# Performance work log

Measured on AMD Instinct MI355X. Metric: run time of the kernel, lower is better.

## Reference

```python
import jax, jax.numpy as jnp
import numpy as np

K = 36  # neighbors

def _gather(points, idx):
    # points: [B,N,C], idx: [B,N,K] -> [B,N,K,C]
    return jax.vmap(lambda p, i: p[i])(points, idx)

def setup_inputs() -> dict:
    key = jax.random.key(0)
    ks = jax.random.split(key, 16)
    B, N, d_points, d_model = 4, 4096, 32, 128
    def lin(k, fan_in, shape):
        return jax.random.normal(k, shape, dtype=jnp.float32) / np.sqrt(fan_in)
    return {
        "features": jax.random.normal(ks[0], (B, N, d_points), dtype=jnp.float32),
        "xyz": jax.random.uniform(ks[1], (B, N, 3), dtype=jnp.float32),
        "W1": lin(ks[2], d_points, (d_model, d_points)), "b1": jnp.zeros((d_model,), jnp.float32),
        "W2": lin(ks[3], d_model, (d_model, d_model)), "b2": jnp.zeros((d_model,), jnp.float32),
        "Wd1": lin(ks[4], 3, (d_model, 3)), "bd1": jnp.zeros((d_model,), jnp.float32),
        "Wd2": lin(ks[5], d_model, (d_model, d_model)), "bd2": jnp.zeros((d_model,), jnp.float32),
        "Wg1": lin(ks[6], d_model, (d_model, d_model)), "bg1": jnp.zeros((d_model,), jnp.float32),
        "Wg2": lin(ks[7], d_model, (d_model, d_model)), "bg2": jnp.zeros((d_model,), jnp.float32),
    }

def reference(features, xyz, W1, b1, W2, b2, Wd1, bd1, Wd2, bd2, Wg1, bg1, Wg2, bg2):
    # square_distance: [B,N,N]
    sq = jnp.sum(xyz * xyz, axis=-1)
    dists = sq[:, :, None] + sq[:, None, :] - 2.0 * jnp.einsum('bnc,bmc->bnm', xyz, xyz)
    knn_idx = jnp.argsort(dists, axis=-1)[:, :, :K]            # [B,N,K]
    knn_xyz = _gather(xyz, knn_idx)                             # [B,N,K,3]
    x = features @ W1.T + b1                                    # [B,N,d]
    k = _gather(x, knn_idx)                                     # [B,N,K,d]
    v = k
    # fc_delta(xyz[:,:,None] - knn_xyz)
    d_in = xyz[:, :, None, :] - knn_xyz                         # [B,N,K,3]
    pos_enc = jax.nn.relu(d_in @ Wd1.T + bd1) @ Wd2.T + bd2     # [B,N,K,d]
    # fc_gamma(q[:,:,None] - k + pos_enc)
    g_in = x[:, :, None, :] - k + pos_enc
    attn_pre = jax.nn.relu(g_in @ Wg1.T + bg1) @ Wg2.T + bg2    # [B,N,K,d]
    attn = jax.nn.softmax(attn_pre / np.sqrt(x.shape[-1]).astype(np.float32), axis=-2)
    res = jnp.einsum('bmnf,bmnf->bmf', attn, v + pos_enc)       # [B,N,d]
    res = res @ W2.T + b2 + x
    return (res, attn)
```

## Files before the change

kernel.cpp:

```cpp
#include <hip/hip_runtime.h>
#include <math.h>

#define BB 4
#define NPT 4096
#define DP 32
#define DD 128
#define KNB 36

typedef unsigned short ushort_t;
typedef unsigned int uint_t;
typedef unsigned long long ull;
typedef __attribute__((ext_vector_type(8))) short bf16x8;
typedef __attribute__((ext_vector_type(4))) float f32x4;

__device__ __forceinline__ ushort_t f2bf(float f) {
    unsigned u = __float_as_uint(f);
    unsigned r = (u + 0x7FFFu + ((u >> 16) & 1u)) >> 16;
    return (ushort_t)r;
}
__device__ __forceinline__ float bf2f(ushort_t h) {
    return __uint_as_float((unsigned)h << 16);
}
__device__ __forceinline__ int swzi(int r, int f) {
    return (r << 7) + (((f >> 3) ^ (r & 15)) << 3) + (f & 7);
}

__global__ __launch_bounds__(256) void k_wcvt(const float* __restrict__ Wd2,
                                              const float* __restrict__ Wg1,
                                              const float* __restrict__ Wg2,
                                              const float* __restrict__ W2,
                                              ushort_t* __restrict__ wb) {
    int i = blockIdx.x * 256 + threadIdx.x;
    wb[i]           = f2bf(Wd2[i]);
    wb[i + 16384]   = f2bf(Wg1[i]);
    wb[i + 32768]   = f2bf(Wg2[i]);
    wb[i + 49152]   = f2bf(W2[i]);
}

__global__ __launch_bounds__(128) void k_x(const float* __restrict__ feat,
                                           const float* __restrict__ xyz,
                                           const float* __restrict__ W1,
                                           const float* __restrict__ b1,
                                           float* __restrict__ x,
                                           float* __restrict__ sq) {
    int row = blockIdx.x;
    int t = threadIdx.x;
    __shared__ float sf[DP];
    if (t < DP) sf[t] = feat[row * DP + t];
    __syncthreads();
    float acc = 0.f;
#pragma unroll
    for (int c = 0; c < DP; ++c) acc = fmaf(sf[c], W1[t * DP + c], acc);
    x[(size_t)row * DD + t] = acc + b1[t];
    if (t == 0) {
        float a = xyz[row * 3 + 0], b = xyz[row * 3 + 1], c = xyz[row * 3 + 2];
        float s = __fadd_rn(__fadd_rn(__fmul_rn(a, a), __fmul_rn(b, b)),
                            __fmul_rn(c, c));
        sq[row] = s;
    }
}

__global__ __launch_bounds__(256) void k_knn2(const float* __restrict__ xyz,
                                              const float* __restrict__ sq,
                                              int* __restrict__ knn) {
    const int row = blockIdx.x;
    const int b = row >> 12;
    const int t = threadIdx.x;
    const int lane = t & 63, wv = t >> 6;

    __shared__ __align__(16) ull cand[2048];
    __shared__ int wsum[4];
    __shared__ ull wred[4];
    __shared__ ull sbest;
    __shared__ int sC, sCnt;

    uint_t* hist4 = (uint_t*)cand;

    const float qx = xyz[row * 3 + 0], qy = xyz[row * 3 + 1], qz = xyz[row * 3 + 2];
    const float qs = sq[row];
    const float* bx = xyz + (size_t)b * NPT * 3;
    const float* bs = sq + (size_t)b * NPT;

#pragma unroll
    for (int i = 0; i < 16; ++i) hist4[t + (i << 8)] = 0;
    if (t == 0) sCnt = 0;
    __syncthreads();

    uint_t k16[16];
#pragma unroll
    for (int i = 0; i < 16; ++i) {
        int m = t + (i << 8);
        float px = bx[m * 3 + 0], py = bx[m * 3 + 1], pz = bx[m * 3 + 2];
        float d0 = __fmul_rn(qx, px);
        float d1 = __fmaf_rn(qy, py, d0);
        float dot = __fmaf_rn(qz, pz, d1);
        float d = __fsub_rn(__fadd_rn(qs, bs[m]), __fmul_rn(2.0f, dot));
        unsigned u = __float_as_uint(d);
        u = (u & 0x80000000u) ? ~u : (u | 0x80000000u);
        k16[i] = u;
        int bin = (u < 0x80000000u) ? 0 : (int)((u - 0x80000000u) >> 21);
        atomicAdd(&hist4[(bin << 2) | (t & 3)], 1u);
    }
    __syncthreads();

    int s_t = 0;
#pragma unroll
    for (int i = 0; i < 16; ++i) s_t += (int)hist4[(t << 4) + i];
    int v = s_t;
    for (int off = 1; off < 64; off <<= 1) {
        int o = __shfl_up(v, off, 64);
        if (lane >= off) v += o;
    }
    if (lane == 63) wsum[wv] = v;
    __syncthreads();
    int base = 0;
    for (int w0 = 0; w0 < wv; ++w0) base += wsum[w0];
    int cumIncl = base + v, cumExcl = cumIncl - s_t;
    if (cumExcl < KNB && cumIncl >= KNB) {
        int run = cumExcl;
#pragma unroll
        for (int j = 0; j < 4; ++j) {
            int bb = (t << 2) + j;
            int h = (int)(hist4[(bb << 2) + 0] + hist4[(bb << 2) + 1] +
                          hist4[(bb << 2) + 2] + hist4[(bb << 2) + 3]);
            if (run + h >= KNB) { sC = bb; break; }
            run += h;
        }
    }
    __syncthreads();
    const int C = sC;

#pragma unroll
    for (int i = 0; i < 16; ++i) {
        uint_t u = k16[i];
        int bin = (u < 0x80000000u) ? 0 : (int)((u - 0x80000000u) >> 21);
        if (bin <= C) {
            int p = atomicAdd(&sCnt, 1);
            if (p < 2048) cand[p] = ((ull)u << 32) | (uint_t)(t + (i << 8));
        }
    }
    __syncthreads();
    const int cnt = sCnt;

    if (cnt <= 64) {
        if (wv == 0) {
            ull x = (lane < cnt) ? cand[lane] : ~0ull;
#pragma unroll
            for (int k = 2; k <= 64; k <<= 1) {
#pragma unroll
                for (int j = k >> 1; j > 0; j >>= 1) {
                    ull o = __shfl_xor(x, j, 64);
                    bool up = ((lane & k) == 0);
                    bool lower = ((lane & j) == 0);
                    ull mn = (x < o) ? x : o;
                    ull mx = (x < o) ? o : x;
                    x = (up == lower) ? mn : mx;
                }
            }
            if (lane < KNB) knn[(size_t)row * KNB + lane] = (int)(x & 0xffffffffu);
        }
        return;
    }

    if (cnt <= 2048) {
        ull lk = ~0ull;
        for (int i = t; i < cnt; i += 256) { ull k = cand[i]; if (k < lk) lk = k; }
        for (int r = 0; r < KNB; ++r) {
            ull k = lk;
#pragma unroll
            for (int off = 32; off >= 1; off >>= 1) {
                ull o = __shfl_down(k, off, 64);
                if (o < k) k = o;
            }
            if (lane == 0) wred[wv] = k;
            __syncthreads();
            if (t == 0) {
                ull best = wred[0];
                for (int w0 = 1; w0 < 4; ++w0) if (wred[w0] < best) best = wred[w0];
                sbest = best;
                knn[(size_t)row * KNB + r] = (int)(best & 0xffffffffu);
            }
            __syncthreads();
            ull best = sbest;
            if (lk == best) {
                for (int i = t; i < cnt; i += 256)
                    if (cand[i] == best) cand[i] = ~0ull;
                ull nm = ~0ull;
                for (int i = t; i < cnt; i += 256) { ull kk = cand[i]; if (kk < nm) nm = kk; }
                lk = nm;
            }
        }
        return;
    }

    {
        uint_t* bm = (uint_t*)cand;
        if (t < 128) bm[t] = 0;
        __syncthreads();
        ull lk = ~0ull;
#pragma unroll
        for (int i = 0; i < 16; ++i) {
            ull k = ((ull)k16[i] << 32) | (uint_t)(t + (i << 8));
            if (k < lk) lk = k;
        }
        for (int r = 0; r < KNB; ++r) {
            ull k = lk;
#pragma unroll
            for (int off = 32; off >= 1; off >>= 1) {
                ull o = __shfl_down(k, off, 64);
                if (o < k) k = o;
            }
            if (lane == 0) wred[wv] = k;
            __syncthreads();
            if (t == 0) {
                ull best = wred[0];
                for (int w0 = 1; w0 < 4; ++w0) if (wred[w0] < best) best = wred[w0];
                sbest = best;
                knn[(size_t)row * KNB + r] = (int)(best & 0xffffffffu);
            }
            __syncthreads();
            ull best = sbest;
            int bi = (int)(best & 0xffffffffu);
            if ((bi & 255) == t) {
                bm[bi >> 5] |= (1u << (bi & 31));
                ull nm = ~0ull;
#pragma unroll
                for (int i = 0; i < 16; ++i) {
                    int m = t + (i << 8);
                    if ((bm[m >> 5] >> (m & 31)) & 1u) continue;
                    ull kk = ((ull)k16[i] << 32) | (uint_t)m;
                    if (kk < nm) nm = kk;
                }
                lk = nm;
            }
        }
    }
}

__global__ __launch_bounds__(256) void k_fused2(
    const float* __restrict__ xyz, const float* __restrict__ x,
    const int* __restrict__ knn,
    const float* __restrict__ Wd1, const float* __restrict__ bd1,
    const float* __restrict__ bd2, const float* __restrict__ bg1,
    const float* __restrict__ bg2, const float* __restrict__ b2,
    const ushort_t* __restrict__ Wd2b, const ushort_t* __restrict__ Wg1b,
    const ushort_t* __restrict__ Wg2b, const ushort_t* __restrict__ W2b,
    float* __restrict__ out_res, float* __restrict__ out_attn) {

    const int p0 = blockIdx.x * 4;
    const int b = p0 >> 12;
    const int t = threadIdx.x;
    const int w = t >> 6;
    const int l = t & 63;

    __shared__ __align__(16) ushort_t Abuf[144 * 128];
    __shared__ __align__(16) ushort_t Vbuf[144 * 128];
    __shared__ float xnb[4 * 128];
    __shared__ float resb[4 * 128];
    __shared__ int sidxb[144];
    __shared__ float dxb[144 * 3];

    if (t < 144) sidxb[t] = knn[(size_t)p0 * KNB + t];
    xnb[t] = x[(size_t)p0 * DD + t];
    xnb[t + 256] = x[(size_t)p0 * DD + t + 256];
    __syncthreads();

    if (t < 144) {
        int g = (t * 456) >> 14;
        int j = sidxb[t];
#pragma unroll
        for (int c = 0; c < 3; ++c)
            dxb[t * 3 + c] = xyz[(size_t)(p0 + g) * 3 + c] - xyz[((size_t)(b << 12) + j) * 3 + c];
    }
    for (int e = t; e < 144 * 32; e += 256) {
        int r = e >> 5, q = e & 31;
        float4 xv = reinterpret_cast<const float4*>(x + ((size_t)(b << 12) + sidxb[r]) * DD)[q];
        int f = q << 2;
        ushort_t* dst = &Vbuf[swzi(r, f)];
        dst[0] = f2bf(xv.x); dst[1] = f2bf(xv.y); dst[2] = f2bf(xv.z); dst[3] = f2bf(xv.w);
    }
    __syncthreads();

    for (int e = t; e < 144 * 128; e += 256) {
        int r = e >> 7, f = e & 127;
        float v = fmaf(Wd1[f * 3 + 0], dxb[r * 3 + 0],
                  fmaf(Wd1[f * 3 + 1], dxb[r * 3 + 1],
                       Wd1[f * 3 + 2] * dxb[r * 3 + 2])) + bd1[f];
        v = fmaxf(v, 0.f);
        Abuf[swzi(r, f)] = f2bf(v);
    }
    __syncthreads();

    const f32x4 z4 = {0.f, 0.f, 0.f, 0.f};

    auto run_gemm = [&](const ushort_t* Wb, f32x4 acc[9][2]) {
        bf16x8 bfrag[2][4];
#pragma unroll
        for (int n2 = 0; n2 < 2; ++n2)
#pragma unroll
            for (int kt = 0; kt < 4; ++kt) {
                int f = ((w * 2 + n2) << 4) + (l & 15);
                int k = (kt << 5) + ((l >> 4) << 3);
                bfrag[n2][kt] = *reinterpret_cast<const bf16x8*>(Wb + f * 128 + k);
            }
#pragma unroll
        for (int mt = 0; mt < 9; ++mt) {
#pragma unroll
            for (int kt = 0; kt < 4; ++kt) {
                int r = (mt << 4) + (l & 15);
                int cs = ((kt << 2) + (l >> 4)) ^ (l & 15);
                bf16x8 a = *reinterpret_cast<const bf16x8*>(&Abuf[(r << 7) + (cs << 3)]);
                acc[mt][0] = __builtin_amdgcn_mfma_f32_16x16x32_bf16(a, bfrag[0][kt], acc[mt][0], 0, 0, 0);
                acc[mt][1] = __builtin_amdgcn_mfma_f32_16x16x32_bf16(a, bfrag[1][kt], acc[mt][1], 0, 0, 0);
            }
        }
    };

    {
        f32x4 acc[9][2];
#pragma unroll
        for (int mt = 0; mt < 9; ++mt) { acc[mt][0] = z4; acc[mt][1] = z4; }
        run_gemm(Wd2b, acc);
        __syncthreads();
#pragma unroll
        for (int mt = 0; mt < 9; ++mt)
#pragma unroll
            for (int n2 = 0; n2 < 2; ++n2) {
                int col = ((w * 2 + n2) << 4) + (l & 15);
#pragma unroll
                for (int rr = 0; rr < 4; ++rr) {
                    int row = (mt << 4) + ((l >> 4) << 2) + rr;
                    int g = (row * 456) >> 14;
                    int vs = swzi(row, col);
                    float pe = acc[mt][n2][rr] + bd2[col];
                    float xk = bf2f(Vbuf[vs]);
                    Vbuf[vs] = f2bf(xk + pe);
                    float gin = (xnb[(g << 7) + col] - xk) + pe;
                    Abuf[swzi(row, col)] = f2bf(gin);
                }
            }
        __syncthreads();
    }

    {
        f32x4 acc[9][2];
#pragma unroll
        for (int mt = 0; mt < 9; ++mt) { acc[mt][0] = z4; acc[mt][1] = z4; }
        run_gemm(Wg1b, acc);
        __syncthreads();
#pragma unroll
        for (int mt = 0; mt < 9; ++mt)
#pragma unroll
            for (int n2 = 0; n2 < 2; ++n2) {
                int col = ((w * 2 + n2) << 4) + (l & 15);
#pragma unroll
                for (int rr = 0; rr < 4; ++rr) {
                    int row = (mt << 4) + ((l >> 4) << 2) + rr;
                    Abuf[swzi(row, col)] = f2bf(fmaxf(acc[mt][n2][rr] + bg1[col], 0.f));
                }
            }
        __syncthreads();
    }

    {
        f32x4 acc[9][2];
#pragma unroll
        for (int mt = 0; mt < 9; ++mt) { acc[mt][0] = z4; acc[mt][1] = z4; }
        run_gemm(Wg2b, acc);
        __syncthreads();
#pragma unroll
        for (int mt = 0; mt < 9; ++mt)
#pragma unroll
            for (int n2 = 0; n2 < 2; ++n2) {
                int col = ((w * 2 + n2) << 4) + (l & 15);
#pragma unroll
                for (int rr = 0; rr < 4; ++rr) {
                    int row = (mt << 4) + ((l >> 4) << 2) + rr;
                    Abuf[swzi(row, col)] = f2bf(acc[mt][n2][rr] + bg2[col]);
                }
            }
        __syncthreads();
    }

    const float sc = 0.08838834764831845f;
#pragma unroll 1
    for (int pp = 0; pp < 2; ++pp) {
        int idx = t + (pp << 8);
        int g = idx >> 7, f = idx & 127;
        int r0 = g * KNB;
        float p[KNB];
        float m = -__builtin_inff();
#pragma unroll
        for (int kk = 0; kk < KNB; ++kk) {
            p[kk] = bf2f(Abuf[swzi(r0 + kk, f)]);
            m = fmaxf(m, p[kk]);
        }
        float sum = 0.f;
#pragma unroll
        for (int kk = 0; kk < KNB; ++kk) {
            float e_ = __expf((p[kk] - m) * sc);
            p[kk] = e_;
            sum += e_;
        }
        float inv = 1.f / sum;
        float ra = 0.f;
        size_t obase = ((size_t)(p0 + g) * KNB) * DD + f;
#pragma unroll
        for (int kk = 0; kk < KNB; ++kk) {
            float a_ = p[kk] * inv;
            out_attn[obase + (size_t)kk * DD] = a_;
            ra = fmaf(a_, bf2f(Vbuf[swzi(r0 + kk, f)]), ra);
        }
        resb[(g << 7) + f] = ra;
    }
    __syncthreads();

    {
        int r = t >> 7, f = t & 127;
        Abuf[swzi(r, f)] = f2bf(resb[t]);
        int t2 = t + 256;
        int r2 = t2 >> 7, f2 = t2 & 127;
        Abuf[swzi(r2, f2)] = f2bf(resb[t2]);
    }
    __syncthreads();

    {
        f32x4 acc0 = z4, acc1 = z4;
#pragma unroll
        for (int kt = 0; kt < 4; ++kt) {
            int r = (l & 15);
            int cs = ((kt << 2) + (l >> 4)) ^ (l & 15);
            bf16x8 a = *reinterpret_cast<const bf16x8*>(&Abuf[(r << 7) + (cs << 3)]);
            int f0 = ((w * 2) << 4) + (l & 15);
            int f1 = ((w * 2 + 1) << 4) + (l & 15);
            int k = (kt << 5) + ((l >> 4) << 3);
            bf16x8 b0 = *reinterpret_cast<const bf16x8*>(W2b + f0 * 128 + k);
            bf16x8 b1 = *reinterpret_cast<const bf16x8*>(W2b + f1 * 128 + k);
            acc0 = __builtin_amdgcn_mfma_f32_16x16x32_bf16(a, b0, acc0, 0, 0, 0);
            acc1 = __builtin_amdgcn_mfma_f32_16x16x32_bf16(a, b1, acc1, 0, 0, 0);
        }
        if ((l >> 4) == 0) {
#pragma unroll
            for (int rr = 0; rr < 4; ++rr) {
                int row = rr;
                int col0 = ((w * 2) << 4) + (l & 15);
                int col1 = ((w * 2 + 1) << 4) + (l & 15);
                out_res[(size_t)(p0 + row) * DD + col0] = acc0[rr] + b2[col0] + xnb[(row << 7) + col0];
                out_res[(size_t)(p0 + row) * DD + col1] = acc1[rr] + b2[col1] + xnb[(row << 7) + col1];
            }
        }
    }
}

extern "C" void kernel_launch(void* const* d_in, const int* in_sizes, int n_in,
                              void* d_out, int out_size, void* d_ws, size_t ws_size,
                              hipStream_t stream) {
    const float* feat = (const float*)d_in[0];
    const float* xyz = (const float*)d_in[1];
    const float* W1 = (const float*)d_in[2];
    const float* b1 = (const float*)d_in[3];
    const float* W2 = (const float*)d_in[4];
    const float* b2 = (const float*)d_in[5];
    const float* Wd1 = (const float*)d_in[6];
    const float* bd1 = (const float*)d_in[7];
    const float* Wd2 = (const float*)d_in[8];
    const float* bd2 = (const float*)d_in[9];
    const float* Wg1 = (const float*)d_in[10];
    const float* bg1 = (const float*)d_in[11];
    const float* Wg2 = (const float*)d_in[12];
    const float* bg2 = (const float*)d_in[13];

    float* out = (float*)d_out;
    float* out_res = out;
    float* out_attn = out + (size_t)BB * NPT * DD;

    float* ws_x = (float*)d_ws;
    float* ws_sq = ws_x + (size_t)BB * NPT * DD;
    int* ws_idx = (int*)(ws_sq + (size_t)BB * NPT);
    ushort_t* wb = (ushort_t*)(ws_idx + (size_t)BB * NPT * KNB);
    ushort_t* Wd2b = wb;
    ushort_t* Wg1b = wb + 16384;
    ushort_t* Wg2b = wb + 32768;
    ushort_t* W2b = wb + 49152;

    hipLaunchKernelGGL(k_wcvt, dim3(64), dim3(256), 0, stream, Wd2, Wg1, Wg2, W2, wb);
    hipLaunchKernelGGL(k_x, dim3(BB * NPT), dim3(128), 0, stream,
                       feat, xyz, W1, b1, ws_x, ws_sq);
    hipLaunchKernelGGL(k_knn2, dim3(BB * NPT), dim3(256), 0, stream,
                       xyz, ws_sq, ws_idx);
    hipLaunchKernelGGL(k_fused2, dim3(BB * NPT / 4), dim3(256), 0, stream,
                       xyz, ws_x, ws_idx, Wd1, bd1, bd2, bg1, bg2, b2,
                       Wd2b, Wg1b, Wg2b, W2b, out_res, out_attn);
}
```

Measured before the change: 369.7 us.

## Halve points per block in fused attention kernel to raise occupancy

The fused kernel now handles 2 query points per block instead of 4. That makes 72 neighbor rows, padded to 80 for MFMA tiles, which roughly halves the shared memory footprint and the accumulator register count. Query features move from shared memory into registers, and the resb staging buffer is removed. The kernel also adds launch_bounds occupancy hints and s_setprio around the MFMA loops. The aim is more resident blocks per CU and better latency hiding, at the cost of padded MFMA work (80 rows for 72) and twice as many blocks, each reloading the weight fragments.

```diff
diff --git a/kernel.cpp b/kernel.cpp
--- a/kernel.cpp
+++ b/kernel.cpp
@@ -237,7 +237,7 @@
     }
 }
 
-__global__ __launch_bounds__(256) void k_fused2(
+__global__ __launch_bounds__(256, 4) void k_fused2(
     const float* __restrict__ xyz, const float* __restrict__ x,
     const int* __restrict__ knn,
     const float* __restrict__ Wd1, const float* __restrict__ bd1,
@@ -247,32 +247,40 @@
     const ushort_t* __restrict__ Wg2b, const ushort_t* __restrict__ W2b,
     float* __restrict__ out_res, float* __restrict__ out_attn) {
 
-    const int p0 = blockIdx.x * 4;
+    const int p0 = blockIdx.x * 2;
     const int b = p0 >> 12;
     const int t = threadIdx.x;
     const int w = t >> 6;
     const int l = t & 63;
 
-    __shared__ __align__(16) ushort_t Abuf[144 * 128];
-    __shared__ __align__(16) ushort_t Vbuf[144 * 128];
-    __shared__ float xnb[4 * 128];
-    __shared__ float resb[4 * 128];
-    __shared__ int sidxb[144];
-    __shared__ float dxb[144 * 3];
-
-    if (t < 144) sidxb[t] = knn[(size_t)p0 * KNB + t];
-    xnb[t] = x[(size_t)p0 * DD + t];
-    xnb[t + 256] = x[(size_t)p0 * DD + t + 256];
-    __syncthreads();
-
-    if (t < 144) {
-        int g = (t * 456) >> 14;
-        int j = sidxb[t];
-#pragma unroll
-        for (int c = 0; c < 3; ++c)
-            dxb[t * 3 + c] = xyz[(size_t)(p0 + g) * 3 + c] - xyz[((size_t)(b << 12) + j) * 3 + c];
-    }
-    for (int e = t; e < 144 * 32; e += 256) {
+    __shared__ __align__(16) ushort_t Abuf[80 * 128];
+    __shared__ __align__(16) ushort_t Vbuf[72 * 128];
+    __shared__ int sidxb[80];
+    __shared__ float dxb[80 * 3];
+
+    const int c0 = ((w * 2) << 4) + (l & 15);
+    const int c1 = ((w * 2 + 1) << 4) + (l & 15);
+    float xn_r[2][2];
+    xn_r[0][0] = x[(size_t)p0 * DD + c0];
+    xn_r[0][1] = x[(size_t)(p0 + 1) * DD + c0];
+    xn_r[1][0] = x[(size_t)p0 * DD + c1];
+    xn_r[1][1] = x[(size_t)(p0 + 1) * DD + c1];
+
+    if (t < 80) sidxb[t] = (t < 72) ? knn[(size_t)p0 * KNB + t] : 0;
+    __syncthreads();
+
+    if (t < 80) {
+        if (t < 72) {
+            int g = (t >= KNB);
+            int j = sidxb[t];
+#pragma unroll
+            for (int c = 0; c < 3; ++c)
+                dxb[t * 3 + c] = xyz[(size_t)(p0 + g) * 3 + c] - xyz[((size_t)(b << 12) + j) * 3 + c];
+        } else {
+            dxb[t * 3 + 0] = 0.f; dxb[t * 3 + 1] = 0.f; dxb[t * 3 + 2] = 0.f;
+        }
+    }
+    for (int e = t; e < 72 * 32; e += 256) {
         int r = e >> 5, q = e & 31;
         float4 xv = reinterpret_cast<const float4*>(x + ((size_t)(b << 12) + sidxb[r]) * DD)[q];
         int f = q << 2;
@@ -281,7 +289,7 @@
     }
     __syncthreads();
 
-    for (int e = t; e < 144 * 128; e += 256) {
+    for (int e = t; e < 80 * 128; e += 256) {
         int r = e >> 7, f = e & 127;
         float v = fmaf(Wd1[f * 3 + 0], dxb[r * 3 + 0],
                   fmaf(Wd1[f * 3 + 1], dxb[r * 3 + 1],
@@ -293,7 +301,7 @@
 
     const f32x4 z4 = {0.f, 0.f, 0.f, 0.f};
 
-    auto run_gemm = [&](const ushort_t* Wb, f32x4 acc[9][2]) {
+    auto run_gemm = [&](const ushort_t* Wb, f32x4 acc[5][2]) {
         bf16x8 bfrag[2][4];
 #pragma unroll
         for (int n2 = 0; n2 < 2; ++n2)
@@ -303,8 +311,9 @@
                 int k = (kt << 5) + ((l >> 4) << 3);
                 bfrag[n2][kt] = *reinterpret_cast<const bf16x8*>(Wb + f * 128 + k);
             }
-#pragma unroll
-        for (int mt = 0; mt < 9; ++mt) {
+        __builtin_amdgcn_s_setprio(1);
+#pragma unroll
+        for (int mt = 0; mt < 5; ++mt) {
 #pragma unroll
             for (int kt = 0; kt < 4; ++kt) {
                 int r = (mt << 4) + (l & 15);
@@ -314,79 +323,83 @@
                 acc[mt][1] = __builtin_amdgcn_mfma_f32_16x16x32_bf16(a, bfrag[1][kt], acc[mt][1], 0, 0, 0);
             }
         }
+        __builtin_amdgcn_s_setprio(0);
     };
 
     {
-        f32x4 acc[9][2];
-#pragma unroll
-        for (int mt = 0; mt < 9; ++mt) { acc[mt][0] = z4; acc[mt][1] = z4; }
+        f32x4 acc[5][2];
+#pragma unroll
+        for (int mt = 0; mt < 5; ++mt) { acc[mt][0] = z4; acc[mt][1] = z4; }
         run_gemm(Wd2b, acc);
         __syncthreads();
 #pragma unroll
-        for (int mt = 0; mt < 9; ++mt)
+        for (int mt = 0; mt < 5; ++mt)
 #pragma unroll
             for (int n2 = 0; n2 < 2; ++n2) {
                 int col = ((w * 2 + n2) << 4) + (l & 15);
 #pragma unroll
                 for (int rr = 0; rr < 4; ++rr) {
                     int row = (mt << 4) + ((l >> 4) << 2) + rr;
-                    int g = (row * 456) >> 14;
-                    int vs = swzi(row, col);
-                    float pe = acc[mt][n2][rr] + bd2[col];
-                    float xk = bf2f(Vbuf[vs]);
-                    Vbuf[vs] = f2bf(xk + pe);
-                    float gin = (xnb[(g << 7) + col] - xk) + pe;
-                    Abuf[swzi(row, col)] = f2bf(gin);
+                    if (row < 72) {
+                        int g = (row >= KNB);
+                        int vs = swzi(row, col);
+                        float pe = acc[mt][n2][rr] + bd2[col];
+                        float xk = bf2f(Vbuf[vs]);
+                        Vbuf[vs] = f2bf(xk + pe);
+                        float gin = (xn_r[n2][g] - xk) + pe;
+                        Abuf[swzi(row, col)] = f2bf(gin);
+                    }
                 }
             }
         __syncthreads();
     }
 
     {
-        f32x4 acc[9][2];
-#pragma unroll
-        for (int mt = 0; mt < 9; ++mt) { acc[mt][0] = z4; acc[mt][1] = z4; }
+        f32x4 acc[5][2];
+#pragma unroll
+        for (int mt = 0; mt < 5; ++mt) { acc[mt][0] = z4; acc[mt][1] = z4; }
         run_gemm(Wg1b, acc);
         __syncthreads();
 #pragma unroll
-        for (int mt = 0; mt < 9; ++mt)
+        for (int mt = 0; mt < 5; ++mt)
 #pragma unroll
             for (int n2 = 0; n2 < 2; ++n2) {
                 int col = ((w * 2 + n2) << 4) + (l & 15);
 #pragma unroll
                 for (int rr = 0; rr < 4; ++rr) {
                     int row = (mt << 4) + ((l >> 4) << 2) + rr;
-                    Abuf[swzi(row, col)] = f2bf(fmaxf(acc[mt][n2][rr] + bg1[col], 0.f));
+                    if (row < 72)
+                        Abuf[swzi(row, col)] = f2bf(fmaxf(acc[mt][n2][rr] + bg1[col], 0.f));
                 }
             }
         __syncthreads();
     }
 
     {
-        f32x4 acc[9][2];
-#pragma unroll
-        for (int mt = 0; mt < 9; ++mt) { acc[mt][0] = z4; acc[mt][1] = z4; }
+        f32x4 acc[5][2];
+#pragma unroll
+        for (int mt = 0; mt < 5; ++mt) { acc[mt][0] = z4; acc[mt][1] = z4; }
         run_gemm(Wg2b, acc);
         __syncthreads();
 #pragma unroll
-        for (int mt = 0; mt < 9; ++mt)
+        for (int mt = 0; mt < 5; ++mt)
 #pragma unroll
             for (int n2 = 0; n2 < 2; ++n2) {
                 int col = ((w * 2 + n2) << 4) + (l & 15);
 #pragma unroll
                 for (int rr = 0; rr < 4; ++rr) {
                     int row = (mt << 4) + ((l >> 4) << 2) + rr;
-                    Abuf[swzi(row, col)] = f2bf(acc[mt][n2][rr] + bg2[col]);
+                    if (row < 72)
+                        Abuf[swzi(row, col)] = f2bf(acc[mt][n2][rr] + bg2[col]);
                 }
             }
         __syncthreads();
     }
 
     const float sc = 0.08838834764831845f;
-#pragma unroll 1
-    for (int pp = 0; pp < 2; ++pp) {
-        int idx = t + (pp << 8);
-        int g = idx >> 7, f = idx & 127;
+    float ra;
+    {
+        int g = t >> 7, f = t & 127;
         int r0 = g * KNB;
         float p[KNB];
         float m = -__builtin_inff();
@@ -403,7 +416,7 @@
             sum += e_;
         }
         float inv = 1.f / sum;
-        float ra = 0.f;
+        ra = 0.f;
         size_t obase = ((size_t)(p0 + g) * KNB) * DD + f;
 #pragma unroll
         for (int kk = 0; kk < KNB; ++kk) {
@@ -411,16 +424,11 @@
             out_attn[obase + (size_t)kk * DD] = a_;
             ra = fmaf(a_, bf2f(Vbuf[swzi(r0 + kk, f)]), ra);
         }
-        resb[(g << 7) + f] = ra;
-    }
-    __syncthreads();
-
-    {
-        int r = t >> 7, f = t & 127;
-        Abuf[swzi(r, f)] = f2bf(resb[t]);
-        int t2 = t + 256;
-        int r2 = t2 >> 7, f2 = t2 & 127;
-        Abuf[swzi(r2, f2)] = f2bf(resb[t2]);
+    }
+    __syncthreads();
+    {
+        int g = t >> 7, f = t & 127;
+        Abuf[swzi(g, f)] = f2bf(ra);
     }
     __syncthreads();
 
@@ -431,22 +439,17 @@
             int r = (l & 15);
             int cs = ((kt << 2) + (l >> 4)) ^ (l & 15);
             bf16x8 a = *reinterpret_cast<const bf16x8*>(&Abuf[(r << 7) + (cs << 3)]);
-            int f0 = ((w * 2) << 4) + (l & 15);
-            int f1 = ((w * 2 + 1) << 4) + (l & 15);
             int k = (kt << 5) + ((l >> 4) << 3);
-            bf16x8 b0 = *reinterpret_cast<const bf16x8*>(W2b + f0 * 128 + k);
-            bf16x8 b1 = *reinterpret_cast<const bf16x8*>(W2b + f1 * 128 + k);
+            bf16x8 b0 = *reinterpret_cast<const bf16x8*>(W2b + c0 * 128 + k);
+            bf16x8 b1 = *reinterpret_cast<const bf16x8*>(W2b + c1 * 128 + k);
             acc0 = __builtin_amdgcn_mfma_f32_16x16x32_bf16(a, b0, acc0, 0, 0, 0);
             acc1 = __builtin_amdgcn_mfma_f32_16x16x32_bf16(a, b1, acc1, 0, 0, 0);
         }
         if ((l >> 4) == 0) {
 #pragma unroll
-            for (int rr = 0; rr < 4; ++rr) {
-                int row = rr;
-                int col0 = ((w * 2) << 4) + (l & 15);
-                int col1 = ((w * 2 + 1) << 4) + (l & 15);
-                out_res[(size_t)(p0 + row) * DD + col0] = acc0[rr] + b2[col0] + xnb[(row << 7) + col0];
-                out_res[(size_t)(p0 + row) * DD + col1] = acc1[rr] + b2[col1] + xnb[(row << 7) + col1];
+            for (int rr = 0; rr < 2; ++rr) {
+                out_res[(size_t)(p0 + rr) * DD + c0] = acc0[rr] + b2[c0] + xn_r[0][rr];
+                out_res[(size_t)(p0 + rr) * DD + c1] = acc1[rr] + b2[c1] + xn_r[1][rr];
             }
         }
     }
@@ -488,7 +491,7 @@
                        feat, xyz, W1, b1, ws_x, ws_sq);
     hipLaunchKernelGGL(k_knn2, dim3(BB * NPT), dim3(256), 0, stream,
                        xyz, ws_sq, ws_idx);
-    hipLaunchKernelGGL(k_fused2, dim3(BB * NPT / 4), dim3(256), 0, stream,
+    hipLaunchKernelGGL(k_fused2, dim3(BB * NPT / 2), dim3(256), 0, stream,
                        xyz, ws_x, ws_idx, Wd1, bd1, bd2, bg1, bg2, b2,
                        Wd2b, Wg1b, Wg2b, W2b, out_res, out_attn);
 }
```

Result: slower. 429.2 us (+16.1%).
